# Optimization experiments

Hardware: AMD Instinct MI355X
Metric: run time of the kernel (lower is better)

Reference implementation:

```python
import jax, jax.numpy as jnp
import numpy as np

D_MODEL = 1024
H = 16
D_K = D_MODEL // H
B, S = 4, 2048


def setup_inputs() -> dict:
    key = jax.random.key(0)
    ks = jax.random.split(key, 12)
    s = 1.0 / np.sqrt(D_MODEL)
    inp = {
        "q": jax.random.normal(ks[0], (B, S, D_MODEL), jnp.float32),
        "k": jax.random.normal(ks[1], (B, S, D_MODEL), jnp.float32),
        "v": jax.random.normal(ks[2], (B, S, D_MODEL), jnp.float32),
        "mask": jax.random.randint(ks[3], (1, 1, S, S), 0, 2, jnp.int32),
        # torch nn.Linear convention: weight [out, in], y = x @ W.T + b
        "w_q": jax.random.uniform(ks[4], (D_MODEL, D_MODEL), jnp.float32, -s, s),
        "b_q": jax.random.uniform(ks[5], (D_MODEL,), jnp.float32, -s, s),
        "w_k": jax.random.uniform(ks[6], (D_MODEL, D_MODEL), jnp.float32, -s, s),
        "b_k": jax.random.uniform(ks[7], (D_MODEL,), jnp.float32, -s, s),
        "w_v": jax.random.uniform(ks[8], (D_MODEL, D_MODEL), jnp.float32, -s, s),
        "b_v": jax.random.uniform(ks[9], (D_MODEL,), jnp.float32, -s, s),
        "w_o": jax.random.uniform(ks[10], (D_MODEL, D_MODEL), jnp.float32, -s, s),
        "b_o": jax.random.uniform(ks[11], (D_MODEL,), jnp.float32, -s, s),
    }
    return inp


def _split_heads(x):
    b, s, _ = x.shape
    return x.reshape(b, s, H, D_K).transpose(0, 2, 1, 3)  # [B,H,S,Dk]


def reference(q, k, v, mask, w_q, b_q, w_k, b_k, w_v, b_v, w_o, b_o):
    query = _split_heads(q @ w_q.T + b_q)
    key = _split_heads(k @ w_k.T + b_k)
    value = _split_heads(v @ w_v.T + b_v)
    scores = jnp.einsum("bhqd,bhkd->bhqk", query, key) / jnp.sqrt(
        jnp.asarray(D_K, query.dtype))
    scores = jnp.where(mask == 0, jnp.asarray(-1e9, scores.dtype), scores)
    attn = jax.nn.softmax(scores, axis=-1)  # dropout p=0 (eval) -> identity
    x = jnp.einsum("bhqk,bhkd->bhqd", attn, value)
    x = x.transpose(0, 2, 1, 3).reshape(q.shape[0], -1, H * D_K)
    return x @ w_o.T + b_o
```

## Files before the change

### kernel.cpp

```cpp
#include <hip/hip_runtime.h>

typedef __bf16 bf16_t;
typedef __bf16 bf16x4 __attribute__((ext_vector_type(4)));
typedef __bf16 bf16x8 __attribute__((ext_vector_type(8)));
typedef float f32x4 __attribute__((ext_vector_type(4)));
typedef float f32x16 __attribute__((ext_vector_type(16)));
typedef unsigned int uint;
typedef uint uint2v __attribute__((ext_vector_type(2)));
typedef uint uint4v __attribute__((ext_vector_type(4)));

#define CSCALE 0.18033688011112042f

static __device__ __forceinline__ bf16_t f2bf(float f) {
  unsigned u = __builtin_bit_cast(unsigned, f);
  u = (u + 0x7fff + ((u >> 16) & 1)) >> 16;
  unsigned short h = (unsigned short)u;
  return __builtin_bit_cast(bf16_t, h);
}
static __device__ __forceinline__ uint cvt_pk(float a, float b) {
  uint r;
  asm("v_cvt_pk_bf16_f32 %0, %1, %2" : "=v"(r) : "v"(a), "v"(b));
  return r;
}

#define GLD_LDS(g, l) \
  __builtin_amdgcn_global_load_lds((const __attribute__((address_space(1))) void*)(g), \
                                   (__attribute__((address_space(3))) void*)(l), 16, 0, 0)
#define VMCNT(n) asm volatile("s_waitcnt vmcnt(" #n ")" ::: "memory")
#define LGKM0() asm volatile("s_waitcnt lgkmcnt(0)" ::: "memory")
#define BARRIER() do { __builtin_amdgcn_s_barrier(); __builtin_amdgcn_sched_barrier(0); } while (0)

__global__ void cvt4_f2b(const float* __restrict__ a, const float* __restrict__ b,
                         const float* __restrict__ c, const float* __restrict__ d,
                         bf16_t* __restrict__ oa, bf16_t* __restrict__ ob,
                         bf16_t* __restrict__ oc, bf16_t* __restrict__ od) {
  int i = blockIdx.x * 256 + threadIdx.x;
  const float* src = a;
  bf16_t* dst = oa;
  int w = i >> 18;
  i &= 262143;
  if (w == 1) { src = b; dst = ob; }
  else if (w == 2) { src = c; dst = oc; }
  else if (w == 3) { src = d; dst = od; }
  const float4 f = reinterpret_cast<const float4*>(src)[i];
  bf16x4 o;
  o[0] = f2bf(f.x); o[1] = f2bf(f.y); o[2] = f2bf(f.z); o[3] = f2bf(f.w);
  reinterpret_cast<bf16x4*>(dst)[i] = o;
}

__global__ void mask_bits_k(const int* __restrict__ m, uint* __restrict__ out) {
  int i = blockIdx.x * 256 + threadIdx.x;
  int q = i & 2047, t = i >> 11;
  const int* mrow = m + (size_t)q * 2048 + t * 32;
  uint bits = 0;
#pragma unroll
  for (int j = 0; j < 16; ++j) {
    int r0 = (j & 3) + 8 * (j >> 2);
    bits |= (mrow[r0] ? 1u : 0u) << j;
    bits |= (mrow[r0 + 4] ? 1u : 0u) << (16 + j);
  }
  out[(size_t)t * 2048 + q] = bits;
}

__global__ __launch_bounds__(256, 2) void qkv_gemm(
    const float* __restrict__ qA, const float* __restrict__ kA, const float* __restrict__ vA,
    const bf16_t* __restrict__ wq, const bf16_t* __restrict__ wk, const bf16_t* __restrict__ wv,
    const float* __restrict__ bq, const float* __restrict__ bk, const float* __restrict__ bv,
    bf16_t* __restrict__ Qp, bf16_t* __restrict__ Kp, bf16_t* __restrict__ Vt) {
  constexpr int K = 1024;
  __shared__ __align__(16) bf16_t AsB[2][128 * 32];
  __shared__ __align__(16) bf16_t BsB[3][256 * 32];
  const int z = blockIdx.z;
  const float* A = (z == 0) ? qA : (z == 1) ? kA : vA;
  const bf16_t* W = (z == 0) ? wq : (z == 1) ? wk : wv;
  const float* bias = (z == 0) ? bq : (z == 1) ? bk : bv;

  const int tid = threadIdx.x;
  const int lane = tid & 63;
  const int wv_ = tid >> 6;
  const int wm = (wv_ & 1) * 64, wn = (wv_ >> 1) * 128;
  const int l15 = lane & 15, lhi = lane >> 4;
  const int bm = blockIdx.x, bn = blockIdx.y;

  const int arow0 = tid >> 3;
  const int acol = tid & 7;
  const float* gA = A + (size_t)(bm * 128 + arow0) * K + acol * 4;
  const int brows = tid >> 2;
  const bf16_t* gB = W + (size_t)(bn * 256 + brows) * K + ((tid & 3) ^ (brows & 3)) * 8;

  f32x4 acc[4][8] = {};
  f32x4 rA0[4], rA1[4];

  auto A_LOAD = [&](int t, f32x4* R) {
#pragma unroll
    for (int L = 0; L < 4; ++L)
      R[L] = *reinterpret_cast<const f32x4*>(gA + (size_t)L * 32 * K + t * 32);
  };
  auto A_WRITE = [&](const f32x4* R, int buf) {
#pragma unroll
    for (int L = 0; L < 4; ++L) {
      int row = arow0 + L * 32;
      uint2v u;
      u[0] = cvt_pk(R[L][0], R[L][1]);
      u[1] = cvt_pk(R[L][2], R[L][3]);
      char* p = (char*)&AsB[buf][0] + row * 64 + (((acol >> 1) ^ (row & 3)) * 16) + (acol & 1) * 8;
      *reinterpret_cast<uint2v*>(p) = u;
    }
  };
  auto B_STAGE = [&](int t, int buf) {
#pragma unroll
    for (int c2 = 0; c2 < 4; ++c2)
      GLD_LDS(gB + (size_t)c2 * 64 * K + t * 32, (char*)&BsB[buf][0] + c2 * 4096 + wv_ * 1024);
  };
  auto COMPUTE = [&](int ba, int bb) {
    bf16x8 af[4], bfv[8];
#pragma unroll
    for (int i = 0; i < 4; ++i) {
      int arow = wm + i * 16 + l15;
      af[i] = *reinterpret_cast<const bf16x8*>(
          (const char*)&AsB[ba][0] + arow * 64 + ((lhi ^ (arow & 3)) * 16));
    }
#pragma unroll
    for (int j = 0; j < 8; ++j) {
      int br = wn + j * 16 + l15;
      bfv[j] = *reinterpret_cast<const bf16x8*>(
          (const char*)&BsB[bb][0] + br * 64 + ((lhi ^ (br & 3)) * 16));
    }
#pragma unroll
    for (int i = 0; i < 4; ++i)
#pragma unroll
      for (int j = 0; j < 8; ++j)
        acc[i][j] = __builtin_amdgcn_mfma_f32_16x16x32_bf16(af[i], bfv[j], acc[i][j], 0, 0, 0);
  };

#define QSTEP(T, RL, RW, BAW, BAC, BBC, BBS) \
  A_LOAD((T) + 2, RL); B_STAGE((T) + 2, BBS); \
  COMPUTE(BAC, BBC); \
  VMCNT(8); \
  A_WRITE(RW, BAW); \
  LGKM0(); BARRIER();

  A_LOAD(0, rA0); B_STAGE(0, 0);
  A_LOAD(1, rA1); B_STAGE(1, 1);
  VMCNT(8);
  A_WRITE(rA0, 0);
  LGKM0(); BARRIER();

#pragma unroll 1
  for (int t6 = 0; t6 < 30; t6 += 6) {
    QSTEP(t6 + 0, rA0, rA1, 1, 0, 0, 2)
    QSTEP(t6 + 1, rA1, rA0, 0, 1, 1, 0)
    QSTEP(t6 + 2, rA0, rA1, 1, 0, 2, 1)
    QSTEP(t6 + 3, rA1, rA0, 0, 1, 0, 2)
    QSTEP(t6 + 4, rA0, rA1, 1, 0, 1, 0)
    QSTEP(t6 + 5, rA1, rA0, 0, 1, 2, 1)
  }
  COMPUTE(0, 0);
  VMCNT(4);
  A_WRITE(rA1, 1);
  VMCNT(0);
  LGKM0(); BARRIER();
  COMPUTE(1, 1);

  if (z == 2) {
    const int b = (bm * 128) >> 11;
    const int s0 = (bm * 128) & 2047;
    bf16_t* vb = Vt + ((size_t)b * 1024 + bn * 256 + wn + l15) * 2048 + s0 + wm + lhi * 4;
#pragma unroll
    for (int j = 0; j < 8; ++j) {
      float bv2 = bias[bn * 256 + wn + j * 16 + l15];
#pragma unroll
      for (int i = 0; i < 4; ++i) {
        bf16x4 pk;
#pragma unroll
        for (int r = 0; r < 4; ++r) pk[r] = f2bf(acc[i][j][r] + bv2);
        *reinterpret_cast<bf16x4*>(vb + (size_t)(j * 16) * 2048 + i * 16) = pk;
      }
    }
  } else {
    bf16_t* O = (z == 0) ? Qp : Kp;
    const float scale = (z == 0) ? CSCALE : 1.0f;
#pragma unroll
    for (int i = 0; i < 4; ++i) {
#pragma unroll
      for (int j = 0; j < 8; ++j) {
        int n = bn * 256 + wn + j * 16 + l15;
        float bv2 = bias[n];
#pragma unroll
        for (int r = 0; r < 4; ++r) {
          int m = bm * 128 + wm + i * 16 + lhi * 4 + r;
          O[(size_t)m * 1024 + n] = f2bf((acc[i][j][r] + bv2) * scale);
        }
      }
    }
  }
#undef QSTEP
}

__global__ __launch_bounds__(256, 2) void gemm_o(
    const bf16_t* __restrict__ A, const bf16_t* __restrict__ Bw,
    const float* __restrict__ bias, float* __restrict__ Cout) {
  constexpr int K = 1024;
  __shared__ __align__(16) bf16_t As[3][128 * 32];
  __shared__ __align__(16) bf16_t Bs[3][256 * 32];
  const int tid = threadIdx.x;
  const int lane = tid & 63;
  const int wv_ = tid >> 6;
  const int wm = (wv_ & 1) * 64, wn = (wv_ >> 1) * 128;
  const int l15 = lane & 15, lhi = lane >> 4;
  const int bm = blockIdx.x, bn = blockIdx.y;
  const int rws = tid >> 2;
  const bf16_t* ga = A + (size_t)(bm * 128 + rws) * K + ((tid & 3) ^ (rws & 3)) * 8;
  const bf16_t* gb = Bw + (size_t)(bn * 256 + rws) * K + ((tid & 3) ^ (rws & 3)) * 8;
  f32x4 acc[4][8] = {};

  auto STAGE = [&](int t, int buf) {
#pragma unroll
    for (int c2 = 0; c2 < 2; ++c2)
      GLD_LDS(ga + (size_t)c2 * 64 * K + t * 32, (char*)&As[buf][0] + c2 * 4096 + wv_ * 1024);
#pragma unroll
    for (int c2 = 0; c2 < 4; ++c2)
      GLD_LDS(gb + (size_t)c2 * 64 * K + t * 32, (char*)&Bs[buf][0] + c2 * 4096 + wv_ * 1024);
  };
  auto COMPUTE = [&](int buf) {
    bf16x8 af[4], bfv[8];
#pragma unroll
    for (int i = 0; i < 4; ++i) {
      int arow = wm + i * 16 + l15;
      af[i] = *reinterpret_cast<const bf16x8*>(
          (const char*)&As[buf][0] + arow * 64 + ((lhi ^ (arow & 3)) * 16));
    }
#pragma unroll
    for (int j = 0; j < 8; ++j) {
      int br = wn + j * 16 + l15;
      bfv[j] = *reinterpret_cast<const bf16x8*>(
          (const char*)&Bs[buf][0] + br * 64 + ((lhi ^ (br & 3)) * 16));
    }
#pragma unroll
    for (int i = 0; i < 4; ++i)
#pragma unroll
      for (int j = 0; j < 8; ++j)
        acc[i][j] = __builtin_amdgcn_mfma_f32_16x16x32_bf16(af[i], bfv[j], acc[i][j], 0, 0, 0);
  };

  STAGE(0, 0);
  STAGE(1, 1);
#pragma unroll 1
  for (int tt = 0; tt < 30; tt += 3) {
    VMCNT(6); BARRIER(); COMPUTE(0); STAGE(tt + 2, 2);
    VMCNT(6); BARRIER(); COMPUTE(1); STAGE(tt + 3, 0);
    VMCNT(6); BARRIER(); COMPUTE(2); STAGE(tt + 4, 1);
  }
  VMCNT(6); BARRIER(); COMPUTE(0);
  VMCNT(0); BARRIER(); COMPUTE(1);

#pragma unroll
  for (int i = 0; i < 4; ++i)
#pragma unroll
    for (int j = 0; j < 8; ++j) {
      int n = bn * 256 + wn + j * 16 + l15;
      float bv2 = bias[n];
#pragma unroll
      for (int r = 0; r < 4; ++r) {
        int m = bm * 128 + wm + i * 16 + lhi * 4 + r;
        Cout[(size_t)m * 1024 + n] = acc[i][j][r] + bv2;
      }
    }
}

static __device__ __forceinline__ f32x16 qk_tile(const bf16_t* Kbuf, const bf16x8 qf[4],
                                                 int l31, int h) {
  f32x16 s = {};
  __builtin_amdgcn_s_setprio(1);
#pragma unroll
  for (int c = 0; c < 4; ++c) {
    bf16x8 kf = *reinterpret_cast<const bf16x8*>(Kbuf + l31 * 72 + h * 8 + 16 * c);
    s = __builtin_amdgcn_mfma_f32_32x32x16_bf16(kf, qf[c], s, 0, 0, 0);
  }
  __builtin_amdgcn_s_setprio(0);
  return s;
}

static __device__ __forceinline__ void softmax_tile(
    const f32x16& sv, uint mb, int h, f32x16& o0, f32x16& o1, f32x16& osum,
    float& mrun, bf16x8& pa0, bf16x8& pa1) {
  const uint mbh = mb >> (h << 4);
  float a0 = fmaxf(fmaxf(sv[0], sv[1]), sv[2]);
  float a1 = fmaxf(fmaxf(sv[3], sv[4]), sv[5]);
  float a2 = fmaxf(fmaxf(sv[6], sv[7]), sv[8]);
  float a3 = fmaxf(fmaxf(sv[9], sv[10]), sv[11]);
  float a4 = fmaxf(fmaxf(sv[12], sv[13]), sv[14]);
  float b0 = fmaxf(fmaxf(a0, a1), a2);
  float mt = fmaxf(fmaxf(b0, fmaxf(a3, a4)), sv[15]);
  if (!__all(mt - mrun <= 8.0f)) {
    float mtf = fmaxf(mt, __shfl_xor(mt, 32));
    float mnew = fmaxf(mrun, mtf);
    float alpha = __builtin_amdgcn_exp2f(mrun - mnew);
#pragma unroll
    for (int r = 0; r < 16; ++r) {
      float ar = __shfl(alpha, (r & 3) + 8 * (r >> 2) + 4 * h);
      o0[r] *= ar; o1[r] *= ar; osum[r] *= ar;
    }
    mrun = mnew;
  }
  float p[16];
#pragma unroll
  for (int r = 0; r < 16; ++r) {
    float pv = __builtin_amdgcn_exp2f(sv[r] - mrun);
    uint smask = (uint)__builtin_amdgcn_sbfe((int)mbh, r, 1);
    p[r] = __builtin_bit_cast(float, __builtin_bit_cast(uint, pv) & smask);
  }
  uint dw[8];
#pragma unroll
  for (int i = 0; i < 8; ++i) dw[i] = cvt_pk(p[2 * i], p[2 * i + 1]);
  uint e0 = (uint)__shfl_xor((int)(h ? dw[0] : dw[2]), 32);
  uint e1 = (uint)__shfl_xor((int)(h ? dw[1] : dw[3]), 32);
  uint e2 = (uint)__shfl_xor((int)(h ? dw[4] : dw[6]), 32);
  uint e3 = (uint)__shfl_xor((int)(h ? dw[5] : dw[7]), 32);
  uint4v ua0 = {h ? e0 : dw[0], h ? e1 : dw[1], h ? dw[2] : e0, h ? dw[3] : e1};
  uint4v ua1 = {h ? e2 : dw[4], h ? e3 : dw[5], h ? dw[6] : e2, h ? dw[7] : e3};
  pa0 = __builtin_bit_cast(bf16x8, ua0);
  pa1 = __builtin_bit_cast(bf16x8, ua1);
}

static __device__ __forceinline__ void pv_tile(const bf16_t* Vbuf, bf16x8 pa0, bf16x8 pa1,
                                               bf16x8 ones, int l31, int h,
                                               f32x16& o0, f32x16& o1, f32x16& osum) {
  bf16x8 v00 = *reinterpret_cast<const bf16x8*>(Vbuf + l31 * 40 + h * 8);
  bf16x8 v01 = *reinterpret_cast<const bf16x8*>(Vbuf + l31 * 40 + 16 + h * 8);
  bf16x8 v10 = *reinterpret_cast<const bf16x8*>(Vbuf + (32 + l31) * 40 + h * 8);
  bf16x8 v11 = *reinterpret_cast<const bf16x8*>(Vbuf + (32 + l31) * 40 + 16 + h * 8);
  __builtin_amdgcn_s_setprio(1);
  o0 = __builtin_amdgcn_mfma_f32_32x32x16_bf16(pa0, v00, o0, 0, 0, 0);
  o0 = __builtin_amdgcn_mfma_f32_32x32x16_bf16(pa1, v01, o0, 0, 0, 0);
  o1 = __builtin_amdgcn_mfma_f32_32x32x16_bf16(pa0, v10, o1, 0, 0, 0);
  o1 = __builtin_amdgcn_mfma_f32_32x32x16_bf16(pa1, v11, o1, 0, 0, 0);
  osum = __builtin_amdgcn_mfma_f32_32x32x16_bf16(pa0, ones, osum, 0, 0, 0);
  osum = __builtin_amdgcn_mfma_f32_32x32x16_bf16(pa1, ones, osum, 0, 0, 0);
  __builtin_amdgcn_s_setprio(0);
}

__global__ __launch_bounds__(256, 4) void attn_kernel(
    const bf16_t* __restrict__ Qp, const bf16_t* __restrict__ Kp,
    const bf16_t* __restrict__ Vt, const uint* __restrict__ maskbits,
    bf16_t* __restrict__ Xb) {
  constexpr int S = 2048, D = 1024;
  __shared__ __align__(16) bf16_t Ks[2][32][72];
  __shared__ __align__(16) bf16_t Vs[2][64][40];
  const int tid = threadIdx.x;
  const int wv_ = tid >> 6, lane = tid & 63;
  const int l31 = lane & 31, h = lane >> 5;
  const int blk = blockIdx.x;
  const int bh = blk & 63, qt4 = blk >> 6;
  const int b = bh >> 4, hd = bh & 15;
  const int q0 = qt4 * 128 + wv_ * 32;

  const int rK = tid >> 3, sK = tid & 7;
  const int rV = tid >> 2, sV = tid & 3;
  const bf16_t* gK = Kp + ((size_t)b * S + rK) * D + hd * 64 + sK * 8;
  const bf16_t* gV = Vt + ((size_t)b * 1024 + hd * 64 + rV) * (size_t)S + sV * 8;
  bf16_t* wK0 = &Ks[0][rK][sK * 8];
  bf16_t* wK1 = &Ks[1][rK][sK * 8];
  bf16_t* wV0 = &Vs[0][rV][sV * 8];
  bf16_t* wV1 = &Vs[1][rV][sV * 8];

  const bf16_t* qbase = Qp + (size_t)(b * S + q0 + l31) * D + hd * 64 + h * 8;
  bf16x8 qf[4];
#pragma unroll
  for (int c = 0; c < 4; ++c)
    qf[c] = *reinterpret_cast<const bf16x8*>(qbase + 16 * c);

  const uint* mbase = maskbits + q0 + l31;

  bf16x8 ones;
#pragma unroll
  for (int i = 0; i < 8; ++i) ones[i] = (bf16_t)1.0f;

  f32x16 o0 = {}, o1 = {}, osum = {};
  float mrun = 0.f;
  bf16x8 pa0, pa1;

  {
    bf16x8 k0 = *reinterpret_cast<const bf16x8*>(gK);
    bf16x8 k1 = *reinterpret_cast<const bf16x8*>(gK + (size_t)32 * D);
    bf16x8 v0 = *reinterpret_cast<const bf16x8*>(gV);
    *reinterpret_cast<bf16x8*>(wK0) = k0;
    *reinterpret_cast<bf16x8*>(wK1) = k1;
    *reinterpret_cast<bf16x8*>(wV0) = v0;
  }
  uint mb0 = mbase[0];
  __syncthreads();
  {
    f32x16 s = qk_tile(&Ks[0][0][0], qf, l31, h);
    softmax_tile(s, mb0, h, o0, o1, osum, mrun, pa0, pa1);
  }

  auto body = [&](int j, bf16_t* wK_st, bf16_t* wV_st, const bf16_t* Kq,
                  const bf16_t* Vp, bool stageK) {
    bf16x8 kreg, vreg;
    if (stageK) kreg = *reinterpret_cast<const bf16x8*>(gK + (size_t)(j + 2) * 32 * D);
    vreg = *reinterpret_cast<const bf16x8*>(gV + (size_t)(j + 1) * 32);
    uint mbn = mbase[(size_t)(j + 1) * 2048];
    f32x16 s = qk_tile(Kq, qf, l31, h);
    pv_tile(Vp, pa0, pa1, ones, l31, h, o0, o1, osum);
    softmax_tile(s, mbn, h, o0, o1, osum, mrun, pa0, pa1);
    if (stageK) *reinterpret_cast<bf16x8*>(wK_st) = kreg;
    *reinterpret_cast<bf16x8*>(wV_st) = vreg;
    __syncthreads();
  };

#pragma unroll 1
  for (int jj = 0; jj < 31; ++jj) {
    const int j = 2 * jj;
    body(j,     wK0, wV1, &Ks[1][0][0], &Vs[0][0][0], true);
    body(j + 1, wK1, wV0, &Ks[0][0][0], &Vs[1][0][0], true);
  }
  body(62, wK0, wV1, &Ks[1][0][0], &Vs[0][0][0], false);
  pv_tile(&Vs[1][0][0], pa0, pa1, ones, l31, h, o0, o1, osum);

  bf16_t* xrow = Xb + (size_t)(b * S + q0) * D + hd * 64 + l31;
#pragma unroll
  for (int r = 0; r < 16; ++r) {
    int qrow = (r & 3) + 8 * (r >> 2) + 4 * h;
    float lr = __builtin_amdgcn_rcpf(osum[r]);
    xrow[(size_t)qrow * D] = f2bf(o0[r] * lr);
    xrow[(size_t)qrow * D + 32] = f2bf(o1[r] * lr);
  }
}

extern "C" void kernel_launch(void* const* d_in, const int* in_sizes, int n_in,
                              void* d_out, int out_size, void* d_ws, size_t ws_size,
                              hipStream_t stream) {
  const float* q = (const float*)d_in[0];
  const float* k = (const float*)d_in[1];
  const float* v = (const float*)d_in[2];
  const int* mask = (const int*)d_in[3];
  const float* w_q = (const float*)d_in[4];
  const float* b_q = (const float*)d_in[5];
  const float* w_k = (const float*)d_in[6];
  const float* b_k = (const float*)d_in[7];
  const float* w_v = (const float*)d_in[8];
  const float* b_v = (const float*)d_in[9];
  const float* w_o = (const float*)d_in[10];
  const float* b_o = (const float*)d_in[11];

  char* ws = (char*)d_ws;
  const size_t SZ = (size_t)8192 * 1024 * 2;
  bf16_t* Qp = (bf16_t*)(ws + 0 * SZ);
  bf16_t* Kp = (bf16_t*)(ws + 1 * SZ);
  bf16_t* Vt = (bf16_t*)(ws + 2 * SZ);
  bf16_t* Xb = (bf16_t*)(ws + 3 * SZ);
  uint* maskB = (uint*)(ws + 4 * SZ);
  bf16_t* wqb = (bf16_t*)(ws + 4 * SZ + 8388608);
  bf16_t* wkb = wqb + 1048576;
  bf16_t* wvb = wkb + 1048576;
  bf16_t* wob = wvb + 1048576;

  cvt4_f2b<<<4096, 256, 0, stream>>>(w_q, w_k, w_v, w_o, wqb, wkb, wvb, wob);
  mask_bits_k<<<512, 256, 0, stream>>>(mask, maskB);

  dim3 g3(64, 4, 3);
  qkv_gemm<<<g3, 256, 0, stream>>>(q, k, v, wqb, wkb, wvb, b_q, b_k, b_v, Qp, Kp, Vt);
  attn_kernel<<<1024, 256, 0, stream>>>(Qp, Kp, Vt, maskB, Xb);
  gemm_o<<<dim3(64, 4), 256, 0, stream>>>(Xb, wob, b_o, (float*)d_out);
}
```

Measured before the change: 243.8 us.

## Replace skewed QK/PV software pipeline with straightforward double-buffered attention loop

Removes the software-pipelined schedule where the PV product of the previous tile overlapped the QK and softmax of the current tile, with K staged two tiles ahead. The new loop does QK, softmax, then PV for the same tile, prefetching only the next K and V tiles into a double buffer. The max is now reduced across half-waves before the rescale check. This simplifies the code and may lower register pressure, but it gives up the overlap between MFMA work and softmax ALU work inside an iteration.

```diff
diff --git a/kernel.cpp b/kernel.cpp
--- a/kernel.cpp
+++ b/kernel.cpp
@@ -268,78 +268,6 @@
     }
 }
 
-static __device__ __forceinline__ f32x16 qk_tile(const bf16_t* Kbuf, const bf16x8 qf[4],
-                                                 int l31, int h) {
-  f32x16 s = {};
-  __builtin_amdgcn_s_setprio(1);
-#pragma unroll
-  for (int c = 0; c < 4; ++c) {
-    bf16x8 kf = *reinterpret_cast<const bf16x8*>(Kbuf + l31 * 72 + h * 8 + 16 * c);
-    s = __builtin_amdgcn_mfma_f32_32x32x16_bf16(kf, qf[c], s, 0, 0, 0);
-  }
-  __builtin_amdgcn_s_setprio(0);
-  return s;
-}
-
-static __device__ __forceinline__ void softmax_tile(
-    const f32x16& sv, uint mb, int h, f32x16& o0, f32x16& o1, f32x16& osum,
-    float& mrun, bf16x8& pa0, bf16x8& pa1) {
-  const uint mbh = mb >> (h << 4);
-  float a0 = fmaxf(fmaxf(sv[0], sv[1]), sv[2]);
-  float a1 = fmaxf(fmaxf(sv[3], sv[4]), sv[5]);
-  float a2 = fmaxf(fmaxf(sv[6], sv[7]), sv[8]);
-  float a3 = fmaxf(fmaxf(sv[9], sv[10]), sv[11]);
-  float a4 = fmaxf(fmaxf(sv[12], sv[13]), sv[14]);
-  float b0 = fmaxf(fmaxf(a0, a1), a2);
-  float mt = fmaxf(fmaxf(b0, fmaxf(a3, a4)), sv[15]);
-  if (!__all(mt - mrun <= 8.0f)) {
-    float mtf = fmaxf(mt, __shfl_xor(mt, 32));
-    float mnew = fmaxf(mrun, mtf);
-    float alpha = __builtin_amdgcn_exp2f(mrun - mnew);
-#pragma unroll
-    for (int r = 0; r < 16; ++r) {
-      float ar = __shfl(alpha, (r & 3) + 8 * (r >> 2) + 4 * h);
-      o0[r] *= ar; o1[r] *= ar; osum[r] *= ar;
-    }
-    mrun = mnew;
-  }
-  float p[16];
-#pragma unroll
-  for (int r = 0; r < 16; ++r) {
-    float pv = __builtin_amdgcn_exp2f(sv[r] - mrun);
-    uint smask = (uint)__builtin_amdgcn_sbfe((int)mbh, r, 1);
-    p[r] = __builtin_bit_cast(float, __builtin_bit_cast(uint, pv) & smask);
-  }
-  uint dw[8];
-#pragma unroll
-  for (int i = 0; i < 8; ++i) dw[i] = cvt_pk(p[2 * i], p[2 * i + 1]);
-  uint e0 = (uint)__shfl_xor((int)(h ? dw[0] : dw[2]), 32);
-  uint e1 = (uint)__shfl_xor((int)(h ? dw[1] : dw[3]), 32);
-  uint e2 = (uint)__shfl_xor((int)(h ? dw[4] : dw[6]), 32);
-  uint e3 = (uint)__shfl_xor((int)(h ? dw[5] : dw[7]), 32);
-  uint4v ua0 = {h ? e0 : dw[0], h ? e1 : dw[1], h ? dw[2] : e0, h ? dw[3] : e1};
-  uint4v ua1 = {h ? e2 : dw[4], h ? e3 : dw[5], h ? dw[6] : e2, h ? dw[7] : e3};
-  pa0 = __builtin_bit_cast(bf16x8, ua0);
-  pa1 = __builtin_bit_cast(bf16x8, ua1);
-}
-
-static __device__ __forceinline__ void pv_tile(const bf16_t* Vbuf, bf16x8 pa0, bf16x8 pa1,
-                                               bf16x8 ones, int l31, int h,
-                                               f32x16& o0, f32x16& o1, f32x16& osum) {
-  bf16x8 v00 = *reinterpret_cast<const bf16x8*>(Vbuf + l31 * 40 + h * 8);
-  bf16x8 v01 = *reinterpret_cast<const bf16x8*>(Vbuf + l31 * 40 + 16 + h * 8);
-  bf16x8 v10 = *reinterpret_cast<const bf16x8*>(Vbuf + (32 + l31) * 40 + h * 8);
-  bf16x8 v11 = *reinterpret_cast<const bf16x8*>(Vbuf + (32 + l31) * 40 + 16 + h * 8);
-  __builtin_amdgcn_s_setprio(1);
-  o0 = __builtin_amdgcn_mfma_f32_32x32x16_bf16(pa0, v00, o0, 0, 0, 0);
-  o0 = __builtin_amdgcn_mfma_f32_32x32x16_bf16(pa1, v01, o0, 0, 0, 0);
-  o1 = __builtin_amdgcn_mfma_f32_32x32x16_bf16(pa0, v10, o1, 0, 0, 0);
-  o1 = __builtin_amdgcn_mfma_f32_32x32x16_bf16(pa1, v11, o1, 0, 0, 0);
-  osum = __builtin_amdgcn_mfma_f32_32x32x16_bf16(pa0, ones, osum, 0, 0, 0);
-  osum = __builtin_amdgcn_mfma_f32_32x32x16_bf16(pa1, ones, osum, 0, 0, 0);
-  __builtin_amdgcn_s_setprio(0);
-}
-
 __global__ __launch_bounds__(256, 4) void attn_kernel(
     const bf16_t* __restrict__ Qp, const bf16_t* __restrict__ Kp,
     const bf16_t* __restrict__ Vt, const uint* __restrict__ maskbits,
@@ -359,10 +287,6 @@
   const int rV = tid >> 2, sV = tid & 3;
   const bf16_t* gK = Kp + ((size_t)b * S + rK) * D + hd * 64 + sK * 8;
   const bf16_t* gV = Vt + ((size_t)b * 1024 + hd * 64 + rV) * (size_t)S + sV * 8;
-  bf16_t* wK0 = &Ks[0][rK][sK * 8];
-  bf16_t* wK1 = &Ks[1][rK][sK * 8];
-  bf16_t* wV0 = &Vs[0][rV][sV * 8];
-  bf16_t* wV1 = &Vs[1][rV][sV * 8];
 
   const bf16_t* qbase = Qp + (size_t)(b * S + q0 + l31) * D + hd * 64 + h * 8;
   bf16x8 qf[4];
@@ -378,46 +302,91 @@
 
   f32x16 o0 = {}, o1 = {}, osum = {};
   float mrun = 0.f;
-  bf16x8 pa0, pa1;
 
   {
-    bf16x8 k0 = *reinterpret_cast<const bf16x8*>(gK);
-    bf16x8 k1 = *reinterpret_cast<const bf16x8*>(gK + (size_t)32 * D);
-    bf16x8 v0 = *reinterpret_cast<const bf16x8*>(gV);
-    *reinterpret_cast<bf16x8*>(wK0) = k0;
-    *reinterpret_cast<bf16x8*>(wK1) = k1;
-    *reinterpret_cast<bf16x8*>(wV0) = v0;
-  }
-  uint mb0 = mbase[0];
-  __syncthreads();
-  {
-    f32x16 s = qk_tile(&Ks[0][0][0], qf, l31, h);
-    softmax_tile(s, mb0, h, o0, o1, osum, mrun, pa0, pa1);
-  }
-
-  auto body = [&](int j, bf16_t* wK_st, bf16_t* wV_st, const bf16_t* Kq,
-                  const bf16_t* Vp, bool stageK) {
+    bf16x8 k0r = *reinterpret_cast<const bf16x8*>(gK);
+    bf16x8 v0r = *reinterpret_cast<const bf16x8*>(gV);
+    *reinterpret_cast<bf16x8*>(&Ks[0][rK][sK * 8]) = k0r;
+    *reinterpret_cast<bf16x8*>(&Vs[0][rV][sV * 8]) = v0r;
+    __syncthreads();
+  }
+
+#pragma unroll 2
+  for (int t = 0; t < 64; ++t) {
+    const int cur = t & 1, nxt = cur ^ 1;
+    const bool pf = (t < 63);
     bf16x8 kreg, vreg;
-    if (stageK) kreg = *reinterpret_cast<const bf16x8*>(gK + (size_t)(j + 2) * 32 * D);
-    vreg = *reinterpret_cast<const bf16x8*>(gV + (size_t)(j + 1) * 32);
-    uint mbn = mbase[(size_t)(j + 1) * 2048];
-    f32x16 s = qk_tile(Kq, qf, l31, h);
-    pv_tile(Vp, pa0, pa1, ones, l31, h, o0, o1, osum);
-    softmax_tile(s, mbn, h, o0, o1, osum, mrun, pa0, pa1);
-    if (stageK) *reinterpret_cast<bf16x8*>(wK_st) = kreg;
-    *reinterpret_cast<bf16x8*>(wV_st) = vreg;
-    __syncthreads();
-  };
-
-#pragma unroll 1
-  for (int jj = 0; jj < 31; ++jj) {
-    const int j = 2 * jj;
-    body(j,     wK0, wV1, &Ks[1][0][0], &Vs[0][0][0], true);
-    body(j + 1, wK1, wV0, &Ks[0][0][0], &Vs[1][0][0], true);
-  }
-  body(62, wK0, wV1, &Ks[1][0][0], &Vs[0][0][0], false);
-  pv_tile(&Vs[1][0][0], pa0, pa1, ones, l31, h, o0, o1, osum);
-
+    if (pf) {
+      kreg = *reinterpret_cast<const bf16x8*>(gK + (size_t)(t + 1) * 32 * D);
+      vreg = *reinterpret_cast<const bf16x8*>(gV + (t + 1) * 32);
+    }
+    uint mbc = mbase[t * 2048];
+    f32x16 s = {};
+    __builtin_amdgcn_s_setprio(1);
+#pragma unroll
+    for (int c = 0; c < 4; ++c) {
+      bf16x8 kf = *reinterpret_cast<const bf16x8*>(&Ks[cur][l31][h * 8 + 16 * c]);
+      s = __builtin_amdgcn_mfma_f32_32x32x16_bf16(kf, qf[c], s, 0, 0, 0);
+    }
+    __builtin_amdgcn_s_setprio(0);
+    const uint mbh = mbc >> (h << 4);
+    float a0 = fmaxf(fmaxf(s[0], s[1]), s[2]);
+    float a1 = fmaxf(fmaxf(s[3], s[4]), s[5]);
+    float a2 = fmaxf(fmaxf(s[6], s[7]), s[8]);
+    float a3 = fmaxf(fmaxf(s[9], s[10]), s[11]);
+    float a4 = fmaxf(fmaxf(s[12], s[13]), s[14]);
+    float b0 = fmaxf(fmaxf(a0, a1), a2);
+    float b1 = fmaxf(a3, a4);
+    float mt = fmaxf(fmaxf(b0, b1), s[15]);
+    mt = fmaxf(mt, __shfl_xor(mt, 32));
+    if (!__all(mt - mrun <= 8.0f)) {
+      float mnew = fmaxf(mrun, mt);
+      float alpha = __builtin_amdgcn_exp2f(mrun - mnew);
+#pragma unroll
+      for (int r = 0; r < 16; ++r) {
+        float ar = __shfl(alpha, (r & 3) + 8 * (r >> 2) + 4 * h);
+        o0[r] *= ar; o1[r] *= ar; osum[r] *= ar;
+      }
+      mrun = mnew;
+    }
+    float p[16];
+#pragma unroll
+    for (int r = 0; r < 16; ++r) {
+      float pv = __builtin_amdgcn_exp2f(s[r] - mrun);
+      uint smask = (uint)__builtin_amdgcn_sbfe((int)mbh, r, 1);
+      p[r] = __builtin_bit_cast(float, __builtin_bit_cast(uint, pv) & smask);
+    }
+    uint dw[8];
+#pragma unroll
+    for (int i = 0; i < 8; ++i) dw[i] = cvt_pk(p[2 * i], p[2 * i + 1]);
+    uint e0 = (uint)__shfl_xor((int)(h ? dw[0] : dw[2]), 32);
+    uint e1 = (uint)__shfl_xor((int)(h ? dw[1] : dw[3]), 32);
+    uint e2 = (uint)__shfl_xor((int)(h ? dw[4] : dw[6]), 32);
+    uint e3 = (uint)__shfl_xor((int)(h ? dw[5] : dw[7]), 32);
+    uint4v ua0 = {h ? e0 : dw[0], h ? e1 : dw[1], h ? dw[2] : e0, h ? dw[3] : e1};
+    uint4v ua1 = {h ? e2 : dw[4], h ? e3 : dw[5], h ? dw[6] : e2, h ? dw[7] : e3};
+    bf16x8 pa0 = __builtin_bit_cast(bf16x8, ua0);
+    bf16x8 pa1 = __builtin_bit_cast(bf16x8, ua1);
+    {
+      bf16x8 v00 = *reinterpret_cast<const bf16x8*>(&Vs[cur][l31][h * 8]);
+      bf16x8 v01 = *reinterpret_cast<const bf16x8*>(&Vs[cur][l31][16 + h * 8]);
+      bf16x8 v10 = *reinterpret_cast<const bf16x8*>(&Vs[cur][32 + l31][h * 8]);
+      bf16x8 v11 = *reinterpret_cast<const bf16x8*>(&Vs[cur][32 + l31][16 + h * 8]);
+      __builtin_amdgcn_s_setprio(1);
+      o0 = __builtin_amdgcn_mfma_f32_32x32x16_bf16(pa0, v00, o0, 0, 0, 0);
+      o0 = __builtin_amdgcn_mfma_f32_32x32x16_bf16(pa1, v01, o0, 0, 0, 0);
+      o1 = __builtin_amdgcn_mfma_f32_32x32x16_bf16(pa0, v10, o1, 0, 0, 0);
+      o1 = __builtin_amdgcn_mfma_f32_32x32x16_bf16(pa1, v11, o1, 0, 0, 0);
+      osum = __builtin_amdgcn_mfma_f32_32x32x16_bf16(pa0, ones, osum, 0, 0, 0);
+      osum = __builtin_amdgcn_mfma_f32_32x32x16_bf16(pa1, ones, osum, 0, 0, 0);
+      __builtin_amdgcn_s_setprio(0);
+    }
+    if (pf) {
+      *reinterpret_cast<bf16x8*>(&Ks[nxt][rK][sK * 8]) = kreg;
+      *reinterpret_cast<bf16x8*>(&Vs[nxt][rV][sV * 8]) = vreg;
+      __syncthreads();
+    }
+  }
   bf16_t* xrow = Xb + (size_t)(b * S + q0) * D + hd * 64 + l31;
 #pragma unroll
   for (int r = 0; r < 16; ++r) {
```

New measurement: 348.8 us. 43.1% more time.
